# Optimization experiments

Hardware: AMD Instinct MI355X
Metric: run time of the kernel (lower is better)

## Reference

```python
import jax, jax.numpy as jnp
import numpy as np
import math

B, SEQ_LEN, LABEL_LEN, PRED_LEN = 32, 512, 256, 256
D_MODEL, N_HEADS, D_FF = 512, 8, 2048
ENC_IN, DEC_IN, C_OUT, MARK = 21, 21, 21, 4
MA_K, E_LAYERS, D_LAYERS, FACTOR = 25, 2, 1, 1
DEC_LEN = LABEL_LEN + PRED_LEN


def moving_mean(x, k):
    # replicate-pad front/back then avg-pool(kernel=k, stride=1); x: [B,L,C]
    pad = (k - 1) // 2
    xp = jnp.concatenate([jnp.repeat(x[:, :1], pad, axis=1), x,
                          jnp.repeat(x[:, -1:], pad, axis=1)], axis=1)
    cs = jnp.cumsum(xp, axis=1)
    cs = jnp.concatenate([jnp.zeros_like(cs[:, :1]), cs], axis=1)
    return (cs[:, k:] - cs[:, :-k]) / k


def series_decomp(x):
    trend = moving_mean(x, MA_K)
    return x - trend, trend


def circ_conv3(x, W):
    # circular-padded Conv1d kernel=3, no bias; x: [B,L,Cin], W: [3,Cin,Cout]
    xp = jnp.concatenate([x[:, -1:], x, x[:, :1]], axis=1)
    return xp[:, :-2] @ W[0] + xp[:, 1:-1] @ W[1] + xp[:, 2:] @ W[2]


def pos_embed(L, d):
    pos = jnp.arange(L, dtype=jnp.float32)[:, None]
    div = jnp.exp(jnp.arange(0, d, 2, dtype=jnp.float32) * (-math.log(10000.0) / d))
    pe = jnp.zeros((L, d), jnp.float32)
    pe = pe.at[:, 0::2].set(jnp.sin(pos * div)).at[:, 1::2].set(jnp.cos(pos * div))
    return pe


def data_embed(x, x_mark, val_W, time_W):
    # TokenEmbedding (circular conv) + TimeFeatureEmbedding (linear) + PositionalEmbedding
    return circ_conv3(x, val_W) + x_mark @ time_W + pos_embed(x.shape[1], D_MODEL)[None]


def autocorrelation(q, k, v):
    # q: [B,L,H,E]; k,v: [B,S,H,E]  -> [B,L,H,E]
    Bq, L, H, E = q.shape
    S = k.shape[1]
    if L > S:
        pad = jnp.zeros((Bq, L - S, H, E), q.dtype)
        k = jnp.concatenate([k, pad], axis=1)
        v = jnp.concatenate([v, pad], axis=1)
    else:
        k, v = k[:, :L], v[:, :L]
    qf = jnp.fft.rfft(q.transpose(0, 2, 3, 1), axis=-1)
    kf = jnp.fft.rfft(k.transpose(0, 2, 3, 1), axis=-1)
    corr = jnp.fft.irfft(qf * jnp.conj(kf), n=L, axis=-1)   # [B,H,E,L]
    vals = v.transpose(0, 2, 3, 1)                          # [B,H,E,L]
    top_k = int(FACTOR * math.log(L))
    mean_corr = corr.mean(axis=(1, 2))                      # [B,L]
    weights, delay = jax.lax.top_k(mean_corr, top_k)        # [B,K]
    w = jax.nn.softmax(weights, axis=-1)
    # gather from doubled values == circular shift by delay
    idx = (jnp.arange(L)[None, None, :] + delay[:, :, None]) % L   # [B,K,L]
    pat = jnp.take_along_axis(vals[:, None], idx[:, :, None, None, :], axis=-1)  # [B,K,H,E,L]
    agg = jnp.einsum('bkhel,bk->bhel', pat, w)
    return agg.transpose(0, 3, 1, 2)


def ac_layer(qx, kx, vx, Wq, Wk, Wv, Wo):
    Bq, L, D = qx.shape
    dk = D // N_HEADS
    q = (qx @ Wq).reshape(Bq, L, N_HEADS, dk)
    k = (kx @ Wk).reshape(Bq, kx.shape[1], N_HEADS, dk)
    v = (vx @ Wv).reshape(Bq, vx.shape[1], N_HEADS, dk)
    return autocorrelation(q, k, v).reshape(Bq, L, D) @ Wo


def ffn(x, W1, W2):
    # Conv1d kernel=1 (no bias) pair == pointwise MLP
    return jax.nn.gelu(x @ W1, approximate=False) @ W2


def seasonal_ln(x, g, b):
    mu = x.mean(-1, keepdims=True)
    var = ((x - mu) ** 2).mean(-1, keepdims=True)
    xh = (x - mu) / jnp.sqrt(var + 1e-5) * g + b
    return xh - xh.mean(axis=1, keepdims=True)


def encoder_layer(x, Wq, Wk, Wv, Wo, W1, W2):
    x = x + ac_layer(x, x, x, Wq, Wk, Wv, Wo)
    x, _ = series_decomp(x)
    y = ffn(x, W1, W2)
    x, _ = series_decomp(x + y)
    return x


def decoder_layer(x, cross, sWq, sWk, sWv, sWo, cWq, cWk, cWv, cWo, W1, W2, trend_W):
    x = x + ac_layer(x, x, x, sWq, sWk, sWv, sWo)
    x, t1 = series_decomp(x)
    x = x + ac_layer(x, cross, cross, cWq, cWk, cWv, cWo)
    x, t2 = series_decomp(x)
    y = ffn(x, W1, W2)
    x, t3 = series_decomp(x + y)
    residual_trend = circ_conv3(t1 + t2 + t3, trend_W)   # [B,L,C_OUT]
    return x, residual_trend


def _forward(x_enc, x_mark_enc, x_dec, x_mark_dec,
             enc_val_W, enc_time_W, enc_Wq, enc_Wk, enc_Wv, enc_Wo, enc_W1, enc_W2,
             enc_norm_g, enc_norm_b, dec_val_W, dec_time_W,
             dec_sWq, dec_sWk, dec_sWv, dec_sWo, dec_cWq, dec_cWk, dec_cWv, dec_cWo,
             dec_W1, dec_W2, dec_trend_W, dec_norm_g, dec_norm_b, proj_W, proj_b):
    mean = jnp.repeat(x_enc.mean(axis=1, keepdims=True), PRED_LEN, axis=1)
    zeros = jnp.zeros((x_dec.shape[0], PRED_LEN, x_dec.shape[2]), x_enc.dtype)
    seasonal_init, trend_init = series_decomp(x_enc)
    trend_init = jnp.concatenate([trend_init[:, -LABEL_LEN:], mean], axis=1)
    seasonal_init = jnp.concatenate([seasonal_init[:, -LABEL_LEN:], zeros], axis=1)
    enc = data_embed(x_enc, x_mark_enc, enc_val_W, enc_time_W)
    for i in range(E_LAYERS):
        enc = encoder_layer(enc, enc_Wq[i], enc_Wk[i], enc_Wv[i], enc_Wo[i], enc_W1[i], enc_W2[i])
    enc = seasonal_ln(enc, enc_norm_g, enc_norm_b)
    dec = data_embed(seasonal_init, x_mark_dec, dec_val_W, dec_time_W)
    trend = trend_init
    for i in range(D_LAYERS):
        dec, rt = decoder_layer(dec, enc, dec_sWq[i], dec_sWk[i], dec_sWv[i], dec_sWo[i],
                                dec_cWq[i], dec_cWk[i], dec_cWv[i], dec_cWo[i],
                                dec_W1[i], dec_W2[i], dec_trend_W[i])
        trend = trend + rt
    dec = seasonal_ln(dec, dec_norm_g, dec_norm_b)
    dec_out = dec @ proj_W + proj_b + trend
    return dec_out[:, -PRED_LEN:]


def setup_inputs() -> dict:
    key = jax.random.key(0)
    it = iter(jax.random.split(key, 40))
    def rn(shape, s=1.0):
        return jax.random.normal(next(it), shape, jnp.float32) * s
    W = 0.02
    return {
        'x_enc': rn((B, SEQ_LEN, ENC_IN)),
        'x_mark_enc': rn((B, SEQ_LEN, MARK)),
        'x_dec': rn((B, DEC_LEN, DEC_IN)),
        'x_mark_dec': rn((B, DEC_LEN, MARK)),
        'enc_val_W': rn((3, ENC_IN, D_MODEL), W),
        'enc_time_W': rn((MARK, D_MODEL), W),
        'enc_Wq': rn((E_LAYERS, D_MODEL, D_MODEL), W),
        'enc_Wk': rn((E_LAYERS, D_MODEL, D_MODEL), W),
        'enc_Wv': rn((E_LAYERS, D_MODEL, D_MODEL), W),
        'enc_Wo': rn((E_LAYERS, D_MODEL, D_MODEL), W),
        'enc_W1': rn((E_LAYERS, D_MODEL, D_FF), W),
        'enc_W2': rn((E_LAYERS, D_FF, D_MODEL), W),
        'enc_norm_g': jnp.ones((D_MODEL,), jnp.float32),
        'enc_norm_b': jnp.zeros((D_MODEL,), jnp.float32),
        'dec_val_W': rn((3, DEC_IN, D_MODEL), W),
        'dec_time_W': rn((MARK, D_MODEL), W),
        'dec_sWq': rn((D_LAYERS, D_MODEL, D_MODEL), W),
        'dec_sWk': rn((D_LAYERS, D_MODEL, D_MODEL), W),
        'dec_sWv': rn((D_LAYERS, D_MODEL, D_MODEL), W),
        'dec_sWo': rn((D_LAYERS, D_MODEL, D_MODEL), W),
        'dec_cWq': rn((D_LAYERS, D_MODEL, D_MODEL), W),
        'dec_cWk': rn((D_LAYERS, D_MODEL, D_MODEL), W),
        'dec_cWv': rn((D_LAYERS, D_MODEL, D_MODEL), W),
        'dec_cWo': rn((D_LAYERS, D_MODEL, D_MODEL), W),
        'dec_W1': rn((D_LAYERS, D_MODEL, D_FF), W),
        'dec_W2': rn((D_LAYERS, D_FF, D_MODEL), W),
        'dec_trend_W': rn((D_LAYERS, 3, D_MODEL, C_OUT), W),
        'dec_norm_g': jnp.ones((D_MODEL,), jnp.float32),
        'dec_norm_b': jnp.zeros((D_MODEL,), jnp.float32),
        'proj_W': rn((D_MODEL, C_OUT), W),
        'proj_b': jnp.zeros((C_OUT,), jnp.float32),
    }


def reference(x_enc, x_mark_enc, x_dec, x_mark_dec,
              enc_val_W, enc_time_W, enc_Wq, enc_Wk, enc_Wv, enc_Wo, enc_W1, enc_W2,
              enc_norm_g, enc_norm_b, dec_val_W, dec_time_W,
              dec_sWq, dec_sWk, dec_sWv, dec_sWo, dec_cWq, dec_cWk, dec_cWv, dec_cWo,
              dec_W1, dec_W2, dec_trend_W, dec_norm_g, dec_norm_b, proj_W, proj_b):
    return _forward(x_enc, x_mark_enc, x_dec, x_mark_dec,
                    enc_val_W, enc_time_W, enc_Wq, enc_Wk, enc_Wv, enc_Wo, enc_W1, enc_W2,
                    enc_norm_g, enc_norm_b, dec_val_W, dec_time_W,
                    dec_sWq, dec_sWk, dec_sWv, dec_sWo, dec_cWq, dec_cWk, dec_cWv, dec_cWo,
                    dec_W1, dec_W2, dec_trend_W, dec_norm_g, dec_norm_b, proj_W, proj_b)
```

## Files before the change

### kernel.cpp

```cpp
#include <hip/hip_runtime.h>


typedef _Float16 h8 __attribute__((ext_vector_type(8)));
typedef _Float16 h4 __attribute__((ext_vector_type(4)));
typedef float f32x4 __attribute__((ext_vector_type(4)));

struct P12 { const float* p[12]; };
struct P4  { const float* p[4]; };

__device__ __forceinline__ float gelu_f(float x){
    return 0.5f * x * (1.0f + erff(x * 0.70710678118654752f));
}

__device__ __forceinline__ void gl_lds(const _Float16* gp, _Float16* lp) {
    __builtin_amdgcn_global_load_lds(
        (const __attribute__((address_space(1))) void*)gp,
        (__attribute__((address_space(3))) void*)lp, 16, 0, 0);
}

__global__ void zero_k(float* __restrict__ p, long n){
    long i = (long)blockIdx.x * 256 + threadIdx.x;
    if (i < n) p[i] = 0.f;
}

template<int EPI, int OUT>
__global__ __launch_bounds__(256)
void hgemm_k(const _Float16* __restrict__ A, int lda, int loA,
             const _Float16* __restrict__ Bm, int ldb, int loB,
             const _Float16* __restrict__ Rc, void* __restrict__ Cv,
             int ldc, int loC, int K, int nph, float osc,
             long sA, long sB, long sC)
{
    __shared__ _Float16 As[128 * 64];
    __shared__ _Float16 Bs[128 * 64];
    const int bz = blockIdx.z;
    const int tid = threadIdx.x, lane = tid & 63, w = tid >> 6;
    const int wr = w >> 1, wc = w & 1;
    const _Float16* Ap = A + bz * sA + (long)(blockIdx.y * 128) * lda;
    const _Float16* Bp = Bm + bz * sB + (long)(blockIdx.x * 128) * ldb;

    const int swz = ((lane & 7) ^ ((lane >> 3) & 7)) * 8;
    const int rsub = w * 32 + (lane >> 3);
    const _Float16* ApT = Ap + (long)rsub * lda + swz;
    const _Float16* BpT = Bp + (long)rsub * ldb + swz;
    _Float16* AsT = As + w * 2048;
    _Float16* BsT = Bs + w * 2048;

    const int tpp = K >> 6;
    const int nkt = tpp * nph;
    f32x4 acc[4][4] = {};

    int p = 0, q = 0;
    for (int kt = 0; kt < nkt; ++kt) {
        const int aoff = q * 64 + (p == 2 ? loA : 0);
        const int boff = q * 64 + (p == 1 ? loB : 0);
        __syncthreads();
#pragma unroll
        for (int i = 0; i < 4; i++) {
            gl_lds(ApT + (long)i * 8 * lda + aoff, AsT + i * 512);
            gl_lds(BpT + (long)i * 8 * ldb + boff, BsT + i * 512);
        }
        __syncthreads();
#pragma unroll
        for (int kk = 0; kk < 2; ++kk) {
            h8 af[4], bf[4];
            const int ks = kk * 4 + (lane >> 4);
#pragma unroll
            for (int m = 0; m < 4; m++) {
                int rowa = wr * 64 + m * 16 + (lane & 15);
                af[m] = *(const h8*)(As + rowa * 64 + ((ks ^ (rowa & 7)) * 8));
                int rowb = wc * 64 + m * 16 + (lane & 15);
                bf[m] = *(const h8*)(Bs + rowb * 64 + ((ks ^ (rowb & 7)) * 8));
            }
#pragma unroll
            for (int m = 0; m < 4; m++)
#pragma unroll
                for (int n = 0; n < 4; n++)
                    acc[m][n] = __builtin_amdgcn_mfma_f32_16x16x32_f16(af[m], bf[n], acc[m][n], 0, 0, 0);
        }
        if (++q == tpp) { q = 0; ++p; }
    }

    const int crow0 = blockIdx.y * 128 + wr * 64 + (lane >> 4) * 4;
    const int ccol0 = blockIdx.x * 128 + wc * 64 + (lane & 15);
    if constexpr (OUT == 0) {
        float* Cp = (float*)Cv + (long)bz * sC;
#pragma unroll
        for (int m = 0; m < 4; m++)
#pragma unroll
            for (int n = 0; n < 4; n++) {
                int col = ccol0 + n * 16;
#pragma unroll
                for (int r2 = 0; r2 < 4; r2++) {
                    long idx = (long)(crow0 + m * 16 + r2) * ldc + col;
                    Cp[idx] = acc[m][n][r2] * osc;
                }
            }
    } else if constexpr (OUT == 1) {
        _Float16* Cp = (_Float16*)Cv + (long)bz * sC;
#pragma unroll
        for (int m = 0; m < 4; m++)
#pragma unroll
            for (int n = 0; n < 4; n++) {
                int col = ccol0 + n * 16;
#pragma unroll
                for (int r2 = 0; r2 < 4; r2++) {
                    int row = crow0 + m * 16 + r2;
                    long base = (long)row * ldc + col;
                    float v = acc[m][n][r2] * osc;
                    if (EPI == 1) {
                        long rb = (long)row * 1024 + col;
                        v += (float)Rc[rb] + (float)Rc[rb + 512];
                    }
                    if (EPI == 2) v = gelu_f(v);
                    _Float16 hi = (_Float16)v;
                    Cp[base] = hi;
                    if (loC >= 0) Cp[base + loC] = (_Float16)(v - (float)hi);
                }
            }
    } else {
        __shared__ float diag[512];
        float* mc = (float*)Cv + (long)bz * sC;
        for (int t = tid; t < 512; t += 256) diag[t] = 0.f;
        __syncthreads();
#pragma unroll
        for (int m = 0; m < 4; m++)
#pragma unroll
            for (int n = 0; n < 4; n++) {
                int col = ccol0 + n * 16;
#pragma unroll
                for (int r2 = 0; r2 < 4; r2++) {
                    int row = crow0 + m * 16 + r2;
                    atomicAdd(&diag[(row - col) & 511], acc[m][n][r2]);
                }
            }
        __syncthreads();
        for (int t = tid; t < 512; t += 256) {
            float v = diag[t];
            if (v != 0.f) atomicAdd(&mc[t], v);
        }
    }
}

__global__ __launch_bounds__(256)
void splitAll_k(P12 ps, _Float16* __restrict__ PA, _Float16* __restrict__ PB)
{
    const int m = blockIdx.y;
    const float* __restrict__ src = ps.p[m];
    _Float16* dst;
    if (m < 4)      dst = PA + (long)(2 * m) * 524288;
    else if (m < 8) dst = PB + (long)(2 * (m - 4)) * 524288;
    else            dst = PB + (long)(2 * (m - 8) + 1) * 524288;
    long t = (long)blockIdx.x * 256 + threadIdx.x;
    long row = t >> 6; int kc = (int)(t & 63) * 8;
    const float4 v0 = *(const float4*)(src + row * 512 + kc);
    const float4 v1 = *(const float4*)(src + row * 512 + kc + 4);
    float vv[8] = {v0.x,v0.y,v0.z,v0.w,v1.x,v1.y,v1.z,v1.w};
    h8 hi, lo;
#pragma unroll
    for (int j = 0; j < 8; j++) {
        float s = vv[j] * 64.f;
        _Float16 h = (_Float16)s;
        hi[j] = h; lo[j] = (_Float16)(s - (float)h);
    }
    *(h8*)(dst + row * 1024 + kc)       = hi;
    *(h8*)(dst + row * 1024 + 512 + kc) = lo;
}

__global__ __launch_bounds__(256)
void convWoAll_k(P4 ps, _Float16* __restrict__ PA)
{
    const int z = blockIdx.z;
    const float* __restrict__ src = ps.p[z];
    _Float16* dst = PA + (long)(2 * z + 1) * 524288;
    __shared__ float t[32][33];
    int k0 = blockIdx.x * 32, n0 = blockIdx.y * 32, tid = threadIdx.x;
#pragma unroll
    for (int i = 0; i < 4; i++) {
        int lin = tid + i * 256; int r = lin >> 5, c = lin & 31;
        t[r][c] = src[(long)(k0 + r) * 512 + n0 + c];
    }
    __syncthreads();
#pragma unroll
    for (int i = 0; i < 4; i++) {
        int lin = tid + i * 256; int n = lin >> 5, k = lin & 31;
        float v = t[k][n] * 64.f;
        _Float16 hi = (_Float16)v;
        long base = (long)(n0 + n) * 1024 + k0 + k;
        dst[base]       = hi;
        dst[base + 512] = (_Float16)(v - (float)hi);
    }
}

__global__ __launch_bounds__(256)
void convW2_k(const float* __restrict__ src, _Float16* __restrict__ dst,
              int N, int K)
{
    __shared__ float t[32][33];
    int k0 = blockIdx.x * 32, n0 = blockIdx.y * 32, tid = threadIdx.x;
#pragma unroll
    for (int i = 0; i < 4; i++) {
        int lin = tid + i * 256; int r = lin >> 5, c = lin & 31;
        t[r][c] = src[(long)(k0 + r) * N + n0 + c];
    }
    __syncthreads();
#pragma unroll
    for (int i = 0; i < 4; i++) {
        int lin = tid + i * 256; int n = lin >> 5, k = lin & 31;
        float v = t[k][n];
        _Float16 hi = (_Float16)v;
        long base = (long)(n0 + n) * 2 * K + k0 + k;
        dst[base]     = hi;
        dst[base + K] = (_Float16)(v - (float)hi);
    }
}

__global__ void convW63_k(const float* __restrict__ W, _Float16* __restrict__ dst)
{
    int i = blockIdx.x * 256 + threadIdx.x;
    int k = i & 511, j = i >> 9;
    float v = (j < 63) ? 64.f * W[(long)(j / 21) * 10752 + (long)k * 21 + (j % 21)] : 0.f;
    _Float16 hi = (_Float16)v;
    dst[(long)j * 1024 + k]       = hi;
    dst[(long)j * 1024 + 512 + k] = (_Float16)(v - (float)hi);
}

__global__ __launch_bounds__(256)
void embed_k(const float* __restrict__ x, const float* __restrict__ mark,
             const float* __restrict__ valW, const float* __restrict__ timeW,
             _Float16* __restrict__ cat)
{
    const int lg = blockIdx.x, dh = blockIdx.y, b = blockIdx.z;
    const int tid = threadIdx.x;
    const int dd = dh * 256 + tid;
    const int l0 = lg * 8;
    __shared__ float xs[10][21];
    __shared__ float mk[8][4];
    if (tid < 210) {
        int r = tid / 21, c = tid % 21;
        int ll = (l0 - 1 + r + 512) & 511;
        xs[r][c] = x[((long)b * 512 + ll) * 21 + c];
    }
    if (tid >= 224 && tid < 256) {
        int t2 = tid - 224, il = t2 >> 2, m = t2 & 3;
        mk[il][m] = mark[((long)b * 512 + l0 + il) * 4 + m];
    }
    __syncthreads();
    float acc[8];
#pragma unroll
    for (int il = 0; il < 8; il++) acc[il] = 0.f;
    for (int t = 0; t < 3; t++)
        for (int c = 0; c < 21; c++) {
            float w = valW[(t * 21 + c) * 512 + dd];
#pragma unroll
            for (int il = 0; il < 8; il++)
                acc[il] = fmaf(xs[il + t][c], w, acc[il]);
        }
    for (int m = 0; m < 4; m++) {
        float w = timeW[m * 512 + dd];
#pragma unroll
        for (int il = 0; il < 8; il++)
            acc[il] = fmaf(mk[il][m], w, acc[il]);
    }
    const float freq = expf((float)(dd & ~1) * (-9.210340371976184f / 512.0f));
#pragma unroll
    for (int il = 0; il < 8; il++) {
        float ang = (float)(l0 + il) * freq;
        float pe = (dd & 1) ? cosf(ang) : sinf(ang);
        float v = acc[il] + pe;
        long row = (long)b * 512 + l0 + il;
        _Float16 hi = (_Float16)v;
        cat[row * 1024 + dd]       = hi;
        cat[row * 1024 + 512 + dd] = (_Float16)(v - (float)hi);
    }
}

template<int TREND>
__global__ __launch_bounds__(256)
void decompW_k(const _Float16* __restrict__ xc, _Float16* __restrict__ outc,
               _Float16* __restrict__ tsc)
{
    long t = (long)blockIdx.x * 256 + threadIdx.x;
    long rowg = t >> 7; int d4 = (int)(t & 127) * 4;
    int lg = (int)(rowg & 63); long b = rowg >> 6;
    const int l0 = lg * 8;
    const _Float16* xb = xc + (b << 19);
    float s[8][4] = {};
    float xo[8][4];
#pragma unroll
    for (int rr = -12; rr <= 19; rr++) {
        int rc = l0 + rr; rc = rc < 0 ? 0 : (rc > 511 ? 511 : rc);
        h4 vh = *(const h4*)(xb + ((long)rc << 10) + d4);
        h4 vl = *(const h4*)(xb + ((long)rc << 10) + 512 + d4);
        float vv[4];
#pragma unroll
        for (int j = 0; j < 4; j++) vv[j] = (float)vh[j] + (float)vl[j];
#pragma unroll
        for (int i = 0; i < 8; i++) {
            if (i >= rr - 12 && i <= rr + 12) {
#pragma unroll
                for (int j = 0; j < 4; j++) s[i][j] += vv[j];
            }
        }
        if (rr >= 0 && rr < 8) {
#pragma unroll
            for (int j = 0; j < 4; j++) xo[rr][j] = vv[j];
        }
    }
#pragma unroll
    for (int i = 0; i < 8; i++) {
        long row = b * 512 + l0 + i;
        float tr[4], ov[4];
#pragma unroll
        for (int j = 0; j < 4; j++) {
            tr[j] = s[i][j] * (1.f / 25.f);
            ov[j] = xo[i][j] - tr[j];
        }
        h4 hi, lo;
#pragma unroll
        for (int j = 0; j < 4; j++) {
            _Float16 h = (_Float16)ov[j];
            hi[j] = h; lo[j] = (_Float16)(ov[j] - (float)h);
        }
        *(h4*)(outc + row * 1024 + d4)       = hi;
        *(h4*)(outc + row * 1024 + 512 + d4) = lo;
        if (TREND) {
            _Float16* tp = tsc + row * 1024 + d4;
            if (TREND == 1) {
                h4 th = *(h4*)tp, tl = *(h4*)(tp + 512);
#pragma unroll
                for (int j = 0; j < 4; j++) tr[j] += (float)th[j] + (float)tl[j];
            }
            h4 th2, tl2;
#pragma unroll
            for (int j = 0; j < 4; j++) {
                _Float16 h = (_Float16)tr[j];
                th2[j] = h; tl2[j] = (_Float16)(tr[j] - (float)h);
            }
            *(h4*)tp         = th2;
            *(h4*)(tp + 512) = tl2;
        }
    }
}

__global__ __launch_bounds__(512)
void meanseq2_k(const float* __restrict__ x, float* __restrict__ xm)
{
    int b = blockIdx.x, tid = threadIdx.x;
    __shared__ float sd[504];
    if (tid < 504) {
        int c = tid % 21, g = tid / 21;
        int l0 = g * 22, l1 = l0 + 22 > 512 ? 512 : l0 + 22;
        const float* xb = x + (long)b * 10752;
        float s = 0.f;
        for (int l = l0; l < l1; l++) s += xb[l * 21 + c];
        sd[tid] = s;
    }
    __syncthreads();
    if (tid < 21) {
        float t = 0.f;
#pragma unroll
        for (int g = 0; g < 24; g++) t += sd[g * 21 + tid];
        xm[b * 21 + tid] = t * (1.f / 512.f);
    }
}

__global__ void prep_k(const float* __restrict__ x, const float* __restrict__ xm,
                       float* __restrict__ sinit, float* __restrict__ tinit, int total)
{
    int i = blockIdx.x * 256 + threadIdx.x;
    if (i >= total) return;
    int c = i % 21, l = (i / 21) % 512, b = i / 10752;
    if (l < 256) {
        int lc = 256 + l;
        float s = 0.f;
        for (int j = -12; j <= 12; j++) {
            int ll = lc + j; ll = ll > 511 ? 511 : ll;
            s += x[((long)b * 512 + ll) * 21 + c];
        }
        float t = s * (1.f / 25.f);
        tinit[i] = t;
        sinit[i] = x[((long)b * 512 + lc) * 21 + c] - t;
    } else {
        sinit[i] = 0.f;
        tinit[i] = xm[b * 21 + c];
    }
}

__global__ __launch_bounds__(256)
void topk_k(float* __restrict__ mc, int* __restrict__ delays,
            float* __restrict__ wts)
{
    const float SCL = 1.f / (512.f * 4096.f);
    int b = blockIdx.x, tid = threadIdx.x;
    __shared__ float v[512];
    __shared__ float rv[256];
    __shared__ int   ri[256];
    __shared__ float selv[6];
    v[tid]       = mc[b * 512 + tid]       * SCL;
    v[tid + 256] = mc[b * 512 + tid + 256] * SCL;
    mc[b * 512 + tid] = 0.f;
    mc[b * 512 + tid + 256] = 0.f;
    __syncthreads();
    for (int p = 0; p < 6; p++) {
        float bv = v[tid]; int bi = tid;
        float v2 = v[tid + 256];
        if (v2 > bv) { bv = v2; bi = tid + 256; }
        rv[tid] = bv; ri[tid] = bi;
        __syncthreads();
        for (int s = 128; s > 0; s >>= 1) {
            if (tid < s) {
                float ov = rv[tid + s]; int oi = ri[tid + s];
                if (ov > rv[tid] || (ov == rv[tid] && oi < ri[tid])) {
                    rv[tid] = ov; ri[tid] = oi;
                }
            }
            __syncthreads();
        }
        if (tid == 0) { selv[p] = rv[0]; delays[b * 6 + p] = ri[0]; v[ri[0]] = -3.4e38f; }
        __syncthreads();
    }
    if (tid == 0) {
        float mx = selv[0];
        for (int p = 1; p < 6; p++) mx = fmaxf(mx, selv[p]);
        float e[6], sum = 0.f;
        for (int p = 0; p < 6; p++) { e[p] = expf(selv[p] - mx); sum += e[p]; }
        for (int p = 0; p < 6; p++) wts[b * 6 + p] = e[p] / sum;
    }
}

__global__ __launch_bounds__(256)
void agg2_k(const _Float16* __restrict__ Vc, int vld,
            const int* __restrict__ delays, const float* __restrict__ wts,
            _Float16* __restrict__ out)
{
    long t = (long)blockIdx.x * 256 + threadIdx.x;
    int dc = (int)(t & 63);
    long row = t >> 6;
    int l = (int)(row & 511), b = (int)(row >> 9);
    float s[8] = {};
#pragma unroll
    for (int k = 0; k < 6; k++) {
        int dl = delays[b * 6 + k];
        float wv = wts[b * 6 + k];
        long sr = ((long)b * 512 + ((l + dl) & 511)) * vld + dc * 8;
        h8 hi8 = *(const h8*)(Vc + sr);
#pragma unroll
        for (int j = 0; j < 8; j++)
            s[j] = fmaf(wv, (float)hi8[j], s[j]);
    }
    h8 ho;
#pragma unroll
    for (int j = 0; j < 8; j++) ho[j] = (_Float16)s[j];
    *(h8*)(out + row * 512 + dc * 8) = ho;
}

__global__ __launch_bounds__(256)
void ln_k(const _Float16* __restrict__ xc, const float* __restrict__ g,
          const float* __restrict__ be, float* __restrict__ out)
{
    int row = blockIdx.x, tid = threadIdx.x;
    const _Float16* xr = xc + ((long)row << 10);
    float v0 = (float)xr[tid]       + (float)xr[tid + 512];
    float v1 = (float)xr[tid + 256] + (float)xr[tid + 768];
    __shared__ float rs[256];
    rs[tid] = v0 + v1; __syncthreads();
    for (int s = 128; s > 0; s >>= 1) { if (tid < s) rs[tid] += rs[tid + s]; __syncthreads(); }
    float mu = rs[0] * (1.f / 512.f);
    __syncthreads();
    float d0 = v0 - mu, d1 = v1 - mu;
    rs[tid] = d0 * d0 + d1 * d1; __syncthreads();
    for (int s = 128; s > 0; s >>= 1) { if (tid < s) rs[tid] += rs[tid + s]; __syncthreads(); }
    float rstd = 1.0f / sqrtf(rs[0] * (1.f / 512.f) + 1e-5f);
    out[((long)row << 9) + tid]       = d0 * rstd * g[tid] + be[tid];
    out[((long)row << 9) + tid + 256] = d1 * rstd * g[tid + 256] + be[tid + 256];
}

__global__ __launch_bounds__(256)
void colsum_k(const float* __restrict__ x, float* __restrict__ cs)
{
    int d = blockIdx.x * 256 + threadIdx.x;
    int b = blockIdx.y;
    const float* xb = x + ((long)b << 18);
    float s = 0.f;
    for (int l = 0; l < 512; l++) s += xb[((long)l << 9) + d];
    cs[((long)b << 9) + d] = s;
}

__global__ __launch_bounds__(256)
void subcolcat_k(const float* __restrict__ x, const float* __restrict__ cs,
                 _Float16* __restrict__ cat)
{
    long t = (long)blockIdx.x * 256 + threadIdx.x;
    long row = t >> 6; int d8 = (int)(t & 63) * 8;
    int b = (int)(row >> 9);
    const float4* c4 = (const float4*)(cs + ((long)b << 9) + d8);
    float4 m0 = c4[0], m1 = c4[1];
    float m[8] = {m0.x,m0.y,m0.z,m0.w,m1.x,m1.y,m1.z,m1.w};
    const float4* xp = (const float4*)(x + row * 512 + d8);
    float4 x0 = xp[0], x1 = xp[1];
    float v[8] = {x0.x,x0.y,x0.z,x0.w,x1.x,x1.y,x1.z,x1.w};
    h8 hi, lo;
#pragma unroll
    for (int j = 0; j < 8; j++) {
        float vv = v[j] - m[j] * (1.f / 512.f);
        _Float16 h = (_Float16)vv;
        hi[j] = h; lo[j] = (_Float16)(vv - (float)h);
    }
    *(h8*)(cat + row * 1024 + d8)       = hi;
    *(h8*)(cat + row * 1024 + 512 + d8) = lo;
}

__global__ void proj_k(const float* __restrict__ x, const float* __restrict__ cs,
                       const float* __restrict__ pw, const float* __restrict__ pb,
                       const float* __restrict__ tinit, const float* __restrict__ H,
                       float* __restrict__ out, int total)
{
    int i = blockIdx.x * 256 + threadIdx.x;
    if (i >= total) return;
    int c = i % 21, l = (i / 21) % 256 + 256, b = i / 5376;
    const float* xr = x + ((long)(b * 512 + l) << 9);
    const float* csb = cs + ((long)b << 9);
    float s = 0.f;
    for (int d = 0; d < 512; d++)
        s = fmaf(xr[d] - csb[d] * (1.f / 512.f), pw[d * 21 + c], s);
    long r = (long)b * 512;
    float trend = tinit[b * 10752 + l * 21 + c]
                + H[(r + ((l + 511) & 511)) * 128 + c]
                + H[(r + l) * 128 + 21 + c]
                + H[(r + ((l + 1) & 511)) * 128 + 42 + c];
    out[i] = s + pb[c] + trend;
}

static void hgemm(int mode, int nph, float osc,
                  const _Float16* A, int lda, int loA,
                  const _Float16* B, int ldb, int loB,
                  const _Float16* Rc, void* C, int ldc, int loC,
                  int K, int M, int N, int batch,
                  long sA, long sB, long sC, hipStream_t st)
{
    dim3 g(N / 128, M / 128, batch), blk(256);
    switch (mode) {
    case 0:  hgemm_k<0,1><<<g,blk,0,st>>>(A,lda,loA,B,ldb,loB,Rc,C,ldc,loC,K,nph,osc,sA,sB,sC); break;
    case 2:  hgemm_k<2,1><<<g,blk,0,st>>>(A,lda,loA,B,ldb,loB,Rc,C,ldc,loC,K,nph,osc,sA,sB,sC); break;
    case 12: hgemm_k<1,1><<<g,blk,0,st>>>(A,lda,loA,B,ldb,loB,Rc,C,ldc,loC,K,nph,osc,sA,sB,sC); break;
    case 11: hgemm_k<0,0><<<g,blk,0,st>>>(A,lda,loA,B,ldb,loB,Rc,C,ldc,loC,K,nph,osc,sA,sB,sC); break;
    default: hgemm_k<0,2><<<g,blk,0,st>>>(A,lda,loA,B,ldb,loB,Rc,C,ldc,loC,K,nph,osc,sA,sB,sC); break;
    }
}

extern "C" void kernel_launch(void* const* d_in, const int* in_sizes, int n_in,
                              void* d_out, int out_size, void* d_ws, size_t ws_size,
                              hipStream_t stream)
{
    const float* x_enc    = (const float*)d_in[0];
    const float* xm_enc   = (const float*)d_in[1];
    const float* xm_dec   = (const float*)d_in[3];
    const float* enc_valW = (const float*)d_in[4];
    const float* enc_timeW= (const float*)d_in[5];
    const float* enc_Wq   = (const float*)d_in[6];
    const float* enc_Wk   = (const float*)d_in[7];
    const float* enc_Wv   = (const float*)d_in[8];
    const float* enc_Wo   = (const float*)d_in[9];
    const float* enc_W1   = (const float*)d_in[10];
    const float* enc_W2   = (const float*)d_in[11];
    const float* enc_g    = (const float*)d_in[12];
    const float* enc_b    = (const float*)d_in[13];
    const float* dec_valW = (const float*)d_in[14];
    const float* dec_timeW= (const float*)d_in[15];
    const float* sWq = (const float*)d_in[16];
    const float* sWk = (const float*)d_in[17];
    const float* sWv = (const float*)d_in[18];
    const float* sWo = (const float*)d_in[19];
    const float* cWq = (const float*)d_in[20];
    const float* cWk = (const float*)d_in[21];
    const float* cWv = (const float*)d_in[22];
    const float* cWo = (const float*)d_in[23];
    const float* dW1 = (const float*)d_in[24];
    const float* dW2 = (const float*)d_in[25];
    const float* dtW = (const float*)d_in[26];
    const float* dec_g = (const float*)d_in[27];
    const float* dec_b = (const float*)d_in[28];
    const float* projW = (const float*)d_in[29];
    const float* projB = (const float*)d_in[30];

    const size_t W_BYTES = 50000000;
    const size_t perB = 8400000;
    int Bc = 32;
    while (Bc > 1 && W_BYTES + (size_t)Bc * perB + (4u << 20) > ws_size) Bc >>= 1;

    char* wp = (char*)d_ws;
    auto alloc = [&](size_t bytes) { char* p = wp; wp += (bytes + 255) & ~(size_t)255; return p; };

    _Float16* Wcat8  = (_Float16*)alloc(8 * 524288 * 2);
    _Float16* encW1C = (_Float16*)alloc(2 * 2097152 * 2);
    _Float16* encW2C = (_Float16*)alloc(2 * 2097152 * 2);
    _Float16* dW1C   = (_Float16*)alloc(2097152 * 2);
    _Float16* dW2C   = (_Float16*)alloc(2097152 * 2);
    _Float16* W63C   = (_Float16*)alloc(131072 * 2);
    _Float16* PA     = (_Float16*)alloc(8 * 524288 * 2);
    _Float16* PB     = (_Float16*)alloc(8 * 524288 * 2);

    const long ROWS = (long)Bc * 512;
    _Float16* cX     = (_Float16*)alloc(ROWS * 1024 * 2);
    _Float16* cO     = (_Float16*)alloc(ROWS * 1024 * 2);
    _Float16* TSc    = (_Float16*)alloc(ROWS * 1024 * 2);
    _Float16* cAgg   = (_Float16*)alloc(ROWS * 512 * 2);
    _Float16* ENCcat = (_Float16*)alloc(ROWS * 1024 * 2);
    _Float16* bigcat = (_Float16*)alloc(ROWS * 2048 * 2);
    float* F       = (float*)alloc(ROWS * 512 * 4);
    float* H       = (float*)alloc(ROWS * 128 * 4);
    float* sinit   = (float*)alloc((long)Bc * 10752 * 4);
    float* tinit   = (float*)alloc((long)Bc * 10752 * 4);
    float* xmean   = (float*)alloc((long)Bc * 21 * 4);
    float* mc      = (float*)alloc((long)Bc * 512 * 4);
    float* cs      = (float*)alloc((long)Bc * 512 * 4);
    float* wts     = (float*)alloc((long)Bc * 6 * 4);
    int*   delays  = (int*)alloc((long)Bc * 6 * 4);

    dim3 cb(256);
    P12 sp;
    sp.p[0] = enc_Wk;  sp.p[1] = enc_Wk + 262144;
    sp.p[2] = sWk;     sp.p[3] = cWk;
    sp.p[4] = enc_Wq;  sp.p[5] = enc_Wq + 262144;
    sp.p[6] = sWq;     sp.p[7] = cWq;
    sp.p[8] = enc_Wv;  sp.p[9] = enc_Wv + 262144;
    sp.p[10] = sWv;    sp.p[11] = cWv;
    P4 op;
    op.p[0] = enc_Wo;  op.p[1] = enc_Wo + 262144;
    op.p[2] = sWo;     op.p[3] = cWo;
    splitAll_k <<<dim3(128,12), cb, 0, stream>>>(sp, PA, PB);
    convWoAll_k<<<dim3(16,16,4), cb, 0, stream>>>(op, PA);
    hgemm(0, 3, 1.f, PA,1024,512, PB,1024,512, nullptr, Wcat8, 1024, 512,
          512, 512, 512, 8, 524288, 524288, 524288, stream);
    for (int L = 0; L < 2; L++) {
        convW2_k<<<dim3(16,64), cb, 0, stream>>>(enc_W1 + (long)L*1048576, encW1C + (long)L*2097152, 2048, 512);
        convW2_k<<<dim3(64,16), cb, 0, stream>>>(enc_W2 + (long)L*1048576, encW2C + (long)L*2097152, 512, 2048);
    }
    convW2_k<<<dim3(16,64), cb, 0, stream>>>(dW1, dW1C, 2048, 512);
    convW2_k<<<dim3(64,16), cb, 0, stream>>>(dW2, dW2C, 512, 2048);
    convW63_k<<<256, cb, 0, stream>>>(dtW, W63C);

    const int M = (int)ROWS;
    const int t21 = Bc * 10752;
    const int gRows = Bc * 128;
    const int gW = Bc * 32;
    const long sCA = 512 * 1024;
    const float IOS = 1.f / 4096.f;

    zero_k<<<(Bc*512 + 255)/256, 256, 0, stream>>>(mc, Bc*512);

    auto attn = [&](const _Float16* cIn, _Float16* cOut,
                    const _Float16* KVcat, int slot) {
        const _Float16* WqkC_ = Wcat8 + (long)(2*slot)     * 524288;
        const _Float16* WvoC_ = Wcat8 + (long)(2*slot + 1) * 524288;
        hgemm(0, 3, 1.f, cIn,1024,512, WqkC_,1024,512, nullptr, bigcat, 1024, 512,
              512, M, 512, 1, 0,0,0, stream);
        hgemm(20, 3, 1.f, bigcat,1024,512, KVcat,1024,512, nullptr, mc, 0, 0,
              512, 512, 512, Bc, sCA, sCA, 512, stream);
        topk_k<<<Bc, 256, 0, stream>>>(mc, delays, wts);
        agg2_k<<<gRows, 256, 0, stream>>>(KVcat, 1024, delays, wts, cAgg);
        hgemm(12, 1, IOS, cAgg,512,0, WvoC_,1024,512, cIn, cOut, 1024, 512,
              512, M, 512, 1, 0,0,0, stream);
    };
    auto ffn = [&](const _Float16* cIn, _Float16* cOut,
                   const _Float16* W1C, const _Float16* W2C) {
        hgemm(2, 1, 1.f, cIn,1024,512, W1C,1024,512, nullptr, bigcat, 2048, -1,
              512, M, 2048, 1, 0,0,0, stream);
        hgemm(12, 1, 1.f, bigcat,2048,0, W2C,4096,2048, cIn, cOut, 1024, 512,
              2048, M, 512, 1, 0,0,0, stream);
    };

    for (int b0 = 0; b0 < 32; b0 += Bc) {
        const float* xe  = x_enc  + (long)b0 * 10752;
        const float* mke = xm_enc + (long)b0 * 2048;
        const float* mkd = xm_dec + (long)b0 * 2048;
        float* outp = (float*)d_out + (long)b0 * 5376;

        meanseq2_k<<<Bc, 512, 0, stream>>>(xe, xmean);
        prep_k    <<<(t21 + 255)/256, 256, 0, stream>>>(xe, xmean, sinit, tinit, t21);

        embed_k<<<dim3(64,2,Bc), 256, 0, stream>>>(xe, mke, enc_valW, enc_timeW, cX);
        for (int L = 0; L < 2; L++) {
            attn(cX, cO, cX, L);
            decompW_k<0><<<gW, 256, 0, stream>>>(cO, cX, nullptr);
            ffn(cX, cO, encW1C + (long)L*2097152, encW2C + (long)L*2097152);
            decompW_k<0><<<gW, 256, 0, stream>>>(cO, cX, nullptr);
        }
        ln_k       <<<Bc*512, 256, 0, stream>>>(cX, enc_g, enc_b, F);
        colsum_k   <<<dim3(2,Bc), 256, 0, stream>>>(F, cs);
        subcolcat_k<<<gRows, 256, 0, stream>>>(F, cs, ENCcat);

        embed_k<<<dim3(64,2,Bc), 256, 0, stream>>>(sinit, mkd, dec_valW, dec_timeW, cX);

        attn(cX, cO, cX, 2);
        decompW_k<2><<<gW, 256, 0, stream>>>(cO, cX, TSc);
        attn(cX, cO, ENCcat, 3);
        decompW_k<1><<<gW, 256, 0, stream>>>(cO, cX, TSc);
        ffn(cX, cO, dW1C, dW2C);
        decompW_k<1><<<gW, 256, 0, stream>>>(cO, cX, TSc);

        hgemm(11, 1, 1.f/64.f, TSc,1024,512, W63C,1024,512, nullptr, H, 128, 0,
              512, M, 128, 1, 0,0,0, stream);
        ln_k    <<<Bc*512, 256, 0, stream>>>(cX, dec_g, dec_b, F);
        colsum_k<<<dim3(2,Bc), 256, 0, stream>>>(F, cs);
        proj_k  <<<(Bc*5376+255)/256, 256, 0, stream>>>(F, cs, projW, projB,
                                                        tinit, H, outp, Bc*5376);
    }
}
```

Before: 2.233 ms.

## Fuse time-delay aggregation into the output-projection GEMM prologue and merge weight conversions

Removes the separate agg2 kernel and its cAgg intermediate buffer. The top-k delay-weighted gather of V is now computed directly while staging the A tile of a new dedicated GEMM kernel that applies the combined Wv·Wo weights and adds the residual. It also merges the six FFN weight conversion launches into one 3D-grid launch and lowers the per-batch workspace estimate. The cost is that each of the four column blocks recomputes the six-tap gather for its rows, and the A tile is filled by register loads instead of async LDS loads.

```diff
diff --git a/kernel.cpp b/kernel.cpp
--- a/kernel.cpp
+++ b/kernel.cpp
@@ -6,6 +6,7 @@
 typedef float f32x4 __attribute__((ext_vector_type(4)));
 
 struct P12 { const float* p[12]; };
+struct P6  { const float* p[6]; };
 struct P4  { const float* p[4]; };
 
 __device__ __forceinline__ float gelu_f(float x){
@@ -143,6 +144,90 @@
 }
 
 __global__ __launch_bounds__(256)
+void hgemmAgg_k(const _Float16* __restrict__ KV,
+                const int* __restrict__ delays, const float* __restrict__ wts,
+                const _Float16* __restrict__ Bm,
+                const _Float16* __restrict__ Rc, _Float16* __restrict__ Cp,
+                float osc)
+{
+    __shared__ _Float16 As[128 * 64];
+    __shared__ _Float16 Bs[128 * 64];
+    const int tid = threadIdx.x, lane = tid & 63, w = tid >> 6;
+    const int wr = w >> 1, wc = w & 1;
+    const _Float16* Bp = Bm + (long)(blockIdx.x * 128) * 1024;
+
+    const int swz = ((lane & 7) ^ ((lane >> 3) & 7)) * 8;
+    const int rsub = w * 32 + (lane >> 3);
+    const _Float16* BpT = Bp + (long)rsub * 1024 + swz;
+    _Float16* BsT = Bs + w * 2048;
+
+    const int rowblk = blockIdx.y * 128;
+    const int b = (rowblk + rsub) >> 9;
+    int dl[6]; float wv[6];
+#pragma unroll
+    for (int k = 0; k < 6; k++) { dl[k] = delays[b * 6 + k]; wv[k] = wts[b * 6 + k]; }
+    const _Float16* KVb = KV + ((long)b << 19);
+
+    f32x4 acc[4][4] = {};
+    for (int q = 0; q < 8; ++q) {
+        const int coff = q * 64 + swz;
+        __syncthreads();
+#pragma unroll
+        for (int i = 0; i < 4; i++) {
+            int l = (rowblk + rsub + i * 8) & 511;
+            float s8[8] = {};
+#pragma unroll
+            for (int k = 0; k < 6; k++) {
+                const h8 v = *(const h8*)(KVb + ((long)((l + dl[k]) & 511) << 10) + coff);
+#pragma unroll
+                for (int j = 0; j < 8; j++) s8[j] = fmaf(wv[k], (float)v[j], s8[j]);
+            }
+            h8 hv;
+#pragma unroll
+            for (int j = 0; j < 8; j++) hv[j] = (_Float16)s8[j];
+            *(h8*)(As + w * 2048 + i * 512 + lane * 8) = hv;
+            gl_lds(BpT + (long)i * 8 * 1024 + q * 64, BsT + i * 512);
+        }
+        __syncthreads();
+#pragma unroll
+        for (int kk = 0; kk < 2; ++kk) {
+            h8 af[4], bf[4];
+            const int ks = kk * 4 + (lane >> 4);
+#pragma unroll
+            for (int m = 0; m < 4; m++) {
+                int rowa = wr * 64 + m * 16 + (lane & 15);
+                af[m] = *(const h8*)(As + rowa * 64 + ((ks ^ (rowa & 7)) * 8));
+                int rowb = wc * 64 + m * 16 + (lane & 15);
+                bf[m] = *(const h8*)(Bs + rowb * 64 + ((ks ^ (rowb & 7)) * 8));
+            }
+#pragma unroll
+            for (int m = 0; m < 4; m++)
+#pragma unroll
+                for (int n = 0; n < 4; n++)
+                    acc[m][n] = __builtin_amdgcn_mfma_f32_16x16x32_f16(af[m], bf[n], acc[m][n], 0, 0, 0);
+        }
+    }
+
+    const int crow0 = rowblk + wr * 64 + (lane >> 4) * 4;
+    const int ccol0 = blockIdx.x * 128 + wc * 64 + (lane & 15);
+#pragma unroll
+    for (int m = 0; m < 4; m++)
+#pragma unroll
+        for (int n = 0; n < 4; n++) {
+            int col = ccol0 + n * 16;
+#pragma unroll
+            for (int r2 = 0; r2 < 4; r2++) {
+                int row = crow0 + m * 16 + r2;
+                long rb = (long)row * 1024 + col;
+                float v = acc[m][n][r2] * osc + (float)Rc[rb] + (float)Rc[rb + 512];
+                _Float16 hi = (_Float16)v;
+                Cp[rb] = hi;
+                Cp[rb + 512] = (_Float16)(v - (float)hi);
+            }
+        }
+}
+
+__global__ __launch_bounds__(256)
 void splitAll_k(P12 ps, _Float16* __restrict__ PA, _Float16* __restrict__ PB)
 {
     const int m = blockIdx.y;
@@ -193,11 +278,20 @@
 }
 
 __global__ __launch_bounds__(256)
-void convW2_k(const float* __restrict__ src, _Float16* __restrict__ dst,
-              int N, int K)
-{
+void convW2All_k(P6 ps, _Float16* __restrict__ encW1C, _Float16* __restrict__ encW2C,
+                 _Float16* __restrict__ dW1C, _Float16* __restrict__ dW2C)
+{
+    const int z = blockIdx.z;
+    const float* __restrict__ src = ps.p[z];
+    _Float16* dst = (z==0) ? encW1C : (z==1) ? encW1C + 2097152 : (z==2) ? dW1C :
+                    (z==3) ? encW2C : (z==4) ? encW2C + 2097152 : dW2C;
+    const bool isW1 = z < 3;
+    const int N = isW1 ? 2048 : 512;
+    const int K = isW1 ? 512 : 2048;
+    int k0 = (isW1 ? blockIdx.x : blockIdx.y) * 32;
+    int n0 = (isW1 ? blockIdx.y : blockIdx.x) * 32;
     __shared__ float t[32][33];
-    int k0 = blockIdx.x * 32, n0 = blockIdx.y * 32, tid = threadIdx.x;
+    int tid = threadIdx.x;
 #pragma unroll
     for (int i = 0; i < 4; i++) {
         int lin = tid + i * 256; int r = lin >> 5, c = lin & 31;
@@ -427,32 +521,6 @@
         for (int p = 0; p < 6; p++) { e[p] = expf(selv[p] - mx); sum += e[p]; }
         for (int p = 0; p < 6; p++) wts[b * 6 + p] = e[p] / sum;
     }
-}
-
-__global__ __launch_bounds__(256)
-void agg2_k(const _Float16* __restrict__ Vc, int vld,
-            const int* __restrict__ delays, const float* __restrict__ wts,
-            _Float16* __restrict__ out)
-{
-    long t = (long)blockIdx.x * 256 + threadIdx.x;
-    int dc = (int)(t & 63);
-    long row = t >> 6;
-    int l = (int)(row & 511), b = (int)(row >> 9);
-    float s[8] = {};
-#pragma unroll
-    for (int k = 0; k < 6; k++) {
-        int dl = delays[b * 6 + k];
-        float wv = wts[b * 6 + k];
-        long sr = ((long)b * 512 + ((l + dl) & 511)) * vld + dc * 8;
-        h8 hi8 = *(const h8*)(Vc + sr);
-#pragma unroll
-        for (int j = 0; j < 8; j++)
-            s[j] = fmaf(wv, (float)hi8[j], s[j]);
-    }
-    h8 ho;
-#pragma unroll
-    for (int j = 0; j < 8; j++) ho[j] = (_Float16)s[j];
-    *(h8*)(out + row * 512 + dc * 8) = ho;
 }
 
 __global__ __launch_bounds__(256)
@@ -585,7 +653,7 @@
     const float* projB = (const float*)d_in[30];
 
     const size_t W_BYTES = 50000000;
-    const size_t perB = 8400000;
+    const size_t perB = 8000000;
     int Bc = 32;
     while (Bc > 1 && W_BYTES + (size_t)Bc * perB + (4u << 20) > ws_size) Bc >>= 1;
 
@@ -605,7 +673,6 @@
     _Float16* cX     = (_Float16*)alloc(ROWS * 1024 * 2);
     _Float16* cO     = (_Float16*)alloc(ROWS * 1024 * 2);
     _Float16* TSc    = (_Float16*)alloc(ROWS * 1024 * 2);
-    _Float16* cAgg   = (_Float16*)alloc(ROWS * 512 * 2);
     _Float16* ENCcat = (_Float16*)alloc(ROWS * 1024 * 2);
     _Float16* bigcat = (_Float16*)alloc(ROWS * 2048 * 2);
     float* F       = (float*)alloc(ROWS * 512 * 4);
@@ -629,17 +696,15 @@
     P4 op;
     op.p[0] = enc_Wo;  op.p[1] = enc_Wo + 262144;
     op.p[2] = sWo;     op.p[3] = cWo;
+    P6 fp;
+    fp.p[0] = enc_W1;  fp.p[1] = enc_W1 + 1048576; fp.p[2] = dW1;
+    fp.p[3] = enc_W2;  fp.p[4] = enc_W2 + 1048576; fp.p[5] = dW2;
     splitAll_k <<<dim3(128,12), cb, 0, stream>>>(sp, PA, PB);
     convWoAll_k<<<dim3(16,16,4), cb, 0, stream>>>(op, PA);
     hgemm(0, 3, 1.f, PA,1024,512, PB,1024,512, nullptr, Wcat8, 1024, 512,
           512, 512, 512, 8, 524288, 524288, 524288, stream);
-    for (int L = 0; L < 2; L++) {
-        convW2_k<<<dim3(16,64), cb, 0, stream>>>(enc_W1 + (long)L*1048576, encW1C + (long)L*2097152, 2048, 512);
-        convW2_k<<<dim3(64,16), cb, 0, stream>>>(enc_W2 + (long)L*1048576, encW2C + (long)L*2097152, 512, 2048);
-    }
-    convW2_k<<<dim3(16,64), cb, 0, stream>>>(dW1, dW1C, 2048, 512);
-    convW2_k<<<dim3(64,16), cb, 0, stream>>>(dW2, dW2C, 512, 2048);
-    convW63_k<<<256, cb, 0, stream>>>(dtW, W63C);
+    convW2All_k<<<dim3(16,64,6), cb, 0, stream>>>(fp, encW1C, encW2C, dW1C, dW2C);
+    convW63_k  <<<256, cb, 0, stream>>>(dtW, W63C);
 
     const int M = (int)ROWS;
     const int t21 = Bc * 10752;
@@ -659,9 +724,8 @@
         hgemm(20, 3, 1.f, bigcat,1024,512, KVcat,1024,512, nullptr, mc, 0, 0,
               512, 512, 512, Bc, sCA, sCA, 512, stream);
         topk_k<<<Bc, 256, 0, stream>>>(mc, delays, wts);
-        agg2_k<<<gRows, 256, 0, stream>>>(KVcat, 1024, delays, wts, cAgg);
-        hgemm(12, 1, IOS, cAgg,512,0, WvoC_,1024,512, cIn, cOut, 1024, 512,
-              512, M, 512, 1, 0,0,0, stream);
+        hgemmAgg_k<<<dim3(4, M/128), 256, 0, stream>>>(KVcat, delays, wts,
+                                                       WvoC_, cIn, cOut, IOS);
     };
     auto ffn = [&](const _Float16* cIn, _Float16* cOut,
                    const _Float16* W1C, const _Float16* W2C) {
```

New measurement: 2.230 ms. No clear change (-0.1%).
